# Optimization experiments

Hardware: AMD Instinct MI355X
Metric: run time of the kernel (lower is better)

Reference implementation:

```python
import jax, jax.numpy as jnp
import numpy as np


def setup_inputs() -> dict:
    key = jax.random.key(0)
    k1, k2 = jax.random.split(key)
    B, S_ENC, S_DEC, D = 8, 4096, 4096, 256
    enc_output = jax.random.normal(k1, (B, S_ENC, D), dtype=jnp.float32)
    dec_output = jax.random.normal(k2, (B, S_DEC, D), dtype=jnp.float32)
    return {"enc_output": enc_output, "dec_output": dec_output}


def reference(enc_output, dec_output):
    # a_t[b, i, j] = <enc[b, i], dec[b, j]>  -> [B, S_enc, S_dec]
    a_t = jnp.einsum('bid,bjd->bij', enc_output, dec_output)
    # softmax over encoder positions (axis=1), matching torch.softmax(a_t, dim=1)
    a_t = jax.nn.softmax(a_t, axis=1)
    # c_t[b, j, d] = sum_i a_t[b, i, j] * enc[b, i, d]  -> [B, S_dec, D]
    c_t = jnp.einsum('bij,bid->bjd', a_t, enc_output)
    return c_t
```

## Files before the change

kernel.cpp:

```cpp
#include <hip/hip_runtime.h>

typedef unsigned short u16;
typedef unsigned int u32;
typedef __attribute__((ext_vector_type(8))) _Float16 half8;
typedef __attribute__((ext_vector_type(16))) float f32x16;

#define MFMA32(A, B, C) __builtin_amdgcn_mfma_f32_32x32x16_f16(A, B, C, 0, 0, 0)

constexpr int BN = 8;
constexpr int S = 4096;
constexpr int D = 256;
constexpr int KB = 32;
constexpr int NT = S / KB;
constexpr int TILE_U16 = KB * D;

__device__ __forceinline__ u32 pk2h(float a, float b) {
  union { _Float16 h[2]; u32 u; } x;
  x.h[0] = (_Float16)a; x.h[1] = (_Float16)b;
  return x.u;
}

__device__ __forceinline__ void gload_lds16(const void* g, void* l) {
  __builtin_amdgcn_global_load_lds((__attribute__((address_space(1))) void*)(void*)g,
                                   (__attribute__((address_space(3))) void*)l, 16, 0, 0);
}

__global__ __launch_bounds__(256) void convert_enc(const float* __restrict__ enc,
                                                   u16* __restrict__ enc_ws,
                                                   u16* __restrict__ encT_ws) {
  const int blk = blockIdx.x;
  const int b = blk & 7;
  const int tp = blk >> 3;
  const int tid = threadIdx.x;

  const float* encb = enc + (size_t)b * S * D;

#pragma unroll
  for (int it = 0; it < 8; ++it) {
    int gg = it * 256 + tid;
    int t = tp * 2 + (gg >> 10);
    int g = gg & 1023;
    int i = g & 31;
    int ch = g >> 5;
    int d0 = ch * 8;
    const float* src = encb + (size_t)(t * 32 + i) * D + d0;
    float4 x = *(const float4*)src;
    float4 y = *(const float4*)(src + 4);
    uint4 o;
    o.x = pk2h(x.x, x.y); o.y = pk2h(x.z, x.w);
    o.z = pk2h(y.x, y.y); o.w = pk2h(y.z, y.w);
    *(uint4*)(enc_ws + (size_t)(b * NT + t) * TILE_U16 + g * 8) = o;
  }

  {
    int t = tp * 2 + (tid >> 7);
    int r = tid & 127;
    int o = r >> 5;
    int e = r & 31;
    int i0 = o * 8;
    int d0 = e * 8;
    float v[8][8];
#pragma unroll
    for (int rr = 0; rr < 8; ++rr) {
      const float* src = encb + (size_t)(t * 32 + i0 + rr) * D + d0;
      *(float4*)&v[rr][0] = *(const float4*)src;
      *(float4*)&v[rr][4] = *(const float4*)(src + 4);
    }
    int dsub = e >> 2;
    u16* dst = encT_ws + (size_t)(b * NT + t) * TILE_U16 + ((dsub * 4 + o) * 32 + (e & 3) * 8) * 8;
#pragma unroll
    for (int k = 0; k < 8; ++k) {
      uint4 q;
      q.x = pk2h(v[0][k], v[1][k]); q.y = pk2h(v[2][k], v[3][k]);
      q.z = pk2h(v[4][k], v[5][k]); q.w = pk2h(v[6][k], v[7][k]);
      *(uint4*)(dst + k * 8) = q;
    }
  }
}

__global__ __launch_bounds__(512, 2) void attn_kernel(const u16* __restrict__ enc_ws,
                                                      const u16* __restrict__ encT_ws,
                                                      const float* __restrict__ dec,
                                                      float* __restrict__ out) {
  __shared__ u16 lds[2][2][2 * TILE_U16];

  const int tid = threadIdx.x;
  const int w = tid >> 6;
  const int wq = w & 3;
  const int kh = w >> 2;
  const int lane = tid & 63;
  const int h = lane >> 5;
  const int l31 = lane & 31;

  const int blk = blockIdx.x;
  const int b = blk & 7;
  const int q0 = (blk >> 3) << 7;
  const int qw = q0 + wq * 32;

  const u16* encb = enc_ws + (size_t)b * NT * TILE_U16;
  const u16* encTb = encT_ws + (size_t)b * NT * TILE_U16;
  const float* decb = dec + (size_t)b * S * D;

  const float LOG2E = 1.4426950408889634f;
  half8 qf[16];
#pragma unroll
  for (int c = 0; c < 16; ++c) {
    const float* p = decb + (size_t)(qw + l31) * D + c * 16 + h * 8;
    float4 x = *(const float4*)p;
    float4 y = *(const float4*)(p + 4);
    union { u32 u[4]; half8 v; } uu;
    uu.u[0] = pk2h(x.x * LOG2E, x.y * LOG2E);
    uu.u[1] = pk2h(x.z * LOG2E, x.w * LOG2E);
    uu.u[2] = pk2h(y.x * LOG2E, y.y * LOG2E);
    uu.u[3] = pk2h(y.z * LOG2E, y.w * LOG2E);
    qf[c] = uu.v;
  }

  auto stage = [&](int buf, int t) {
    const u16* gimg = (wq < 2) ? (encb + (size_t)t * TILE_U16)
                               : (encTb + (size_t)t * TILE_U16);
    char* limg = (char*)&lds[kh][buf][(wq < 2) ? 0 : TILE_U16];
    const int half = (wq & 1) * 8192;
#pragma unroll
    for (int it = 0; it < 8; ++it) {
      int off = half + it * 1024;
      gload_lds16((const char*)gimg + off + lane * 16, limg + off);
    }
  };

  f32x16 acc[8] = {};
  float mrun = -1e30f;
  float lrun = 0.f;

  stage(0, kh);
  __syncthreads();

  for (int j = 0; j < NT / 2; ++j) {
    const int cur = j & 1;
    if (j + 1 < NT / 2) stage(cur ^ 1, 2 * (j + 1) + kh);

    f32x16 s0 = {}, s1 = {};
    const char* eb = (const char*)&lds[kh][cur][0];
#pragma unroll
    for (int c = 0; c < 16; c += 2) {
      half8 a0 = *(const half8*)(eb + ((c + 0) * 2 + h) * 512 + l31 * 16);
      half8 a1 = *(const half8*)(eb + ((c + 1) * 2 + h) * 512 + l31 * 16);
      s0 = MFMA32(a0, qf[c + 0], s0);
      s1 = MFMA32(a1, qf[c + 1], s1);
    }
    f32x16 st = s0 + s1;

    float x0 = fmaxf(st[0], st[1]), x1 = fmaxf(st[2], st[3]);
    float x2 = fmaxf(st[4], st[5]), x3 = fmaxf(st[6], st[7]);
    float x4 = fmaxf(st[8], st[9]), x5 = fmaxf(st[10], st[11]);
    float x6 = fmaxf(st[12], st[13]), x7 = fmaxf(st[14], st[15]);
    x0 = fmaxf(x0, x1); x2 = fmaxf(x2, x3); x4 = fmaxf(x4, x5); x6 = fmaxf(x6, x7);
    x0 = fmaxf(x0, x2); x4 = fmaxf(x4, x6);
    float tm = fmaxf(x0, x4);
    tm = fmaxf(tm, __shfl_xor(tm, 32));
    if (__any(tm > mrun + 11.5f)) {
      float mnew = fmaxf(mrun, tm);
      float alpha = __builtin_amdgcn_exp2f(mrun - mnew);
      mrun = mnew;
      lrun *= alpha;
#pragma unroll
      for (int ds = 0; ds < 8; ++ds)
#pragma unroll
        for (int r = 0; r < 16; ++r) acc[ds][r] *= alpha;
    }
    float p[16];
#pragma unroll
    for (int r = 0; r < 16; ++r) p[r] = __builtin_amdgcn_exp2f(st[r] - mrun);
    float y0 = (p[0] + p[1]) + (p[2] + p[3]);
    float y1 = (p[4] + p[5]) + (p[6] + p[7]);
    float y2 = (p[8] + p[9]) + (p[10] + p[11]);
    float y3 = (p[12] + p[13]) + (p[14] + p[15]);
    float rs = (y0 + y1) + (y2 + y3);
    rs += __shfl_xor(rs, 32);
    lrun += rs;

    u32 pkw[8];
#pragma unroll
    for (int rq = 0; rq < 4; ++rq) {
      pkw[rq * 2 + 0] = pk2h(p[rq * 4 + 0], p[rq * 4 + 1]);
      pkw[rq * 2 + 1] = pk2h(p[rq * 4 + 2], p[rq * 4 + 3]);
    }
    half8 bfr[2];
#pragma unroll
    for (int ic = 0; ic < 2; ++ic) {
      u32 own0 = pkw[(2 * ic + h) * 2 + 0];
      u32 own1 = pkw[(2 * ic + h) * 2 + 1];
      u32 send0 = pkw[(2 * ic + 1 - h) * 2 + 0];
      u32 send1 = pkw[(2 * ic + 1 - h) * 2 + 1];
      u32 r0 = (u32)__shfl_xor((int)send0, 32);
      u32 r1 = (u32)__shfl_xor((int)send1, 32);
      union { u32 u[4]; half8 v; } bb;
      bb.u[0] = h ? r0 : own0;
      bb.u[1] = h ? r1 : own1;
      bb.u[2] = h ? own0 : r0;
      bb.u[3] = h ? own1 : r1;
      bfr[ic] = bb.v;
    }

    const char* tb = (const char*)&lds[kh][cur][TILE_U16];
#pragma unroll
    for (int ic = 0; ic < 2; ++ic) {
#pragma unroll
      for (int ds = 0; ds < 8; ++ds) {
        half8 vf = *(const half8*)(tb + ((ds * 2 + ic) * 2 + h) * 512 + l31 * 16);
        acc[ds] = MFMA32(vf, bfr[ic], acc[ds]);
      }
    }

    __syncthreads();
  }

  float* fb = (float*)&lds[0][0][0];
  constexpr int XS = 20;
  float* mlb = fb + 30208;

  if (kh == 1) {
    if (lane < 32) {
      mlb[wq * 64 + lane] = mrun;
      mlb[wq * 64 + 32 + lane] = lrun;
    }
#pragma unroll
    for (int d4 = 0; d4 < 4; ++d4) {
      float* dst = fb + ((wq * 4 + d4) * 64 + lane) * XS;
#pragma unroll
      for (int r4 = 0; r4 < 4; ++r4) {
        float4 v;
        v.x = acc[d4][r4 * 4 + 0]; v.y = acc[d4][r4 * 4 + 1];
        v.z = acc[d4][r4 * 4 + 2]; v.w = acc[d4][r4 * 4 + 3];
        *(float4*)(dst + r4 * 4) = v;
      }
    }
  }
  __syncthreads();

  float a0 = 0.f, a1 = 0.f, inv = 0.f;
  const int q = qw + l31;
  float* orow = out + ((size_t)(b * S + q)) * D;
  if (kh == 0) {
    float m1 = mlb[wq * 64 + l31];
    float l1 = mlb[wq * 64 + 32 + l31];
    float mn = fmaxf(mrun, m1);
    a0 = __builtin_amdgcn_exp2f(mrun - mn);
    a1 = __builtin_amdgcn_exp2f(m1 - mn);
    inv = 1.0f / (a0 * lrun + a1 * l1);
#pragma unroll
    for (int d4 = 0; d4 < 4; ++d4) {
      const float* src = fb + ((wq * 4 + d4) * 64 + lane) * XS;
#pragma unroll
      for (int rq = 0; rq < 4; ++rq) {
        float4 u = *(const float4*)(src + rq * 4);
        int d = d4 * 32 + rq * 8 + h * 4;
        float4 o;
        o.x = (a0 * acc[d4][rq * 4 + 0] + a1 * u.x) * inv;
        o.y = (a0 * acc[d4][rq * 4 + 1] + a1 * u.y) * inv;
        o.z = (a0 * acc[d4][rq * 4 + 2] + a1 * u.z) * inv;
        o.w = (a0 * acc[d4][rq * 4 + 3] + a1 * u.w) * inv;
        *(float4*)(orow + d) = o;
      }
    }
  }
  __syncthreads();

  if (kh == 1) {
#pragma unroll
    for (int d4 = 0; d4 < 4; ++d4) {
      float* dst = fb + ((wq * 4 + d4) * 64 + lane) * XS;
#pragma unroll
      for (int r4 = 0; r4 < 4; ++r4) {
        float4 v;
        v.x = acc[d4 + 4][r4 * 4 + 0]; v.y = acc[d4 + 4][r4 * 4 + 1];
        v.z = acc[d4 + 4][r4 * 4 + 2]; v.w = acc[d4 + 4][r4 * 4 + 3];
        *(float4*)(dst + r4 * 4) = v;
      }
    }
  }
  __syncthreads();

  if (kh == 0) {
#pragma unroll
    for (int d4 = 0; d4 < 4; ++d4) {
      const float* src = fb + ((wq * 4 + d4) * 64 + lane) * XS;
#pragma unroll
      for (int rq = 0; rq < 4; ++rq) {
        float4 u = *(const float4*)(src + rq * 4);
        int d = (d4 + 4) * 32 + rq * 8 + h * 4;
        float4 o;
        o.x = (a0 * acc[d4 + 4][rq * 4 + 0] + a1 * u.x) * inv;
        o.y = (a0 * acc[d4 + 4][rq * 4 + 1] + a1 * u.y) * inv;
        o.z = (a0 * acc[d4 + 4][rq * 4 + 2] + a1 * u.z) * inv;
        o.w = (a0 * acc[d4 + 4][rq * 4 + 3] + a1 * u.w) * inv;
        *(float4*)(orow + d) = o;
      }
    }
  }
}

extern "C" void kernel_launch(void* const* d_in, const int* in_sizes, int n_in,
                              void* d_out, int out_size, void* d_ws, size_t ws_size,
                              hipStream_t stream) {
  const float* enc = (const float*)d_in[0];
  const float* dec = (const float*)d_in[1];
  float* out = (float*)d_out;

  u16* enc_ws = (u16*)d_ws;
  u16* encT_ws = enc_ws + (size_t)BN * NT * TILE_U16;

  convert_enc<<<BN * (S / 64), 256, 0, stream>>>(enc, enc_ws, encT_ws);
  attn_kernel<<<BN * (S / 128), 512, 0, stream>>>(enc_ws, encT_ws, dec, out);
}
```

Measured before the change: 186.9 us.

## Split key range across separate blocks with atomic-flag merge of partial softmax

```diff
diff --git a/kernel.cpp b/kernel.cpp
--- a/kernel.cpp
+++ b/kernel.cpp
@@ -13,6 +13,13 @@
 constexpr int KB = 32;
 constexpr int NT = S / KB;
 constexpr int TILE_U16 = KB * D;
+constexpr int TP_U16 = 2 * TILE_U16;
+
+constexpr size_t WS_IMG_BYTES = (size_t)BN * NT * TP_U16 * 2;
+constexpr size_t WS_ML_OFF = WS_IMG_BYTES;
+constexpr size_t WS_ML_BYTES = 256 * 128 * 8;
+constexpr size_t WS_FLAG_OFF = WS_ML_OFF + WS_ML_BYTES;
+constexpr size_t WS_NEED = WS_FLAG_OFF + 2 * 256 * 4;
 
 __device__ __forceinline__ u32 pk2h(float a, float b) {
   union { _Float16 h[2]; u32 u; } x;
@@ -26,8 +33,7 @@
 }
 
 __global__ __launch_bounds__(256) void convert_enc(const float* __restrict__ enc,
-                                                   u16* __restrict__ enc_ws,
-                                                   u16* __restrict__ encT_ws) {
+                                                   u16* __restrict__ ws) {
   const int blk = blockIdx.x;
   const int b = blk & 7;
   const int tp = blk >> 3;
@@ -49,7 +55,7 @@
     uint4 o;
     o.x = pk2h(x.x, x.y); o.y = pk2h(x.z, x.w);
     o.z = pk2h(y.x, y.y); o.w = pk2h(y.z, y.w);
-    *(uint4*)(enc_ws + (size_t)(b * NT + t) * TILE_U16 + g * 8) = o;
+    *(uint4*)(ws + (size_t)(b * NT + t) * TP_U16 + g * 8) = o;
   }
 
   {
@@ -66,8 +72,10 @@
       *(float4*)&v[rr][0] = *(const float4*)src;
       *(float4*)&v[rr][4] = *(const float4*)(src + 4);
     }
-    int dsub = e >> 2;
-    u16* dst = encT_ws + (size_t)(b * NT + t) * TILE_U16 + ((dsub * 4 + o) * 32 + (e & 3) * 8) * 8;
+    int dsub = e >> 4;
+    dsub = e >> 2;
+    u16* dst = ws + (size_t)(b * NT + t) * TP_U16 + TILE_U16 +
+               ((dsub * 4 + o) * 32 + (e & 3) * 8) * 8;
 #pragma unroll
     for (int k = 0; k < 8; ++k) {
       uint4 q;
@@ -78,27 +86,30 @@
   }
 }
 
-__global__ __launch_bounds__(512, 2) void attn_kernel(const u16* __restrict__ enc_ws,
-                                                      const u16* __restrict__ encT_ws,
-                                                      const float* __restrict__ dec,
-                                                      float* __restrict__ out) {
-  __shared__ u16 lds[2][2][2 * TILE_U16];
+__global__ __launch_bounds__(256, 2) void attn_split(const u16* __restrict__ ws_img,
+                                                     const float* __restrict__ dec,
+                                                     float* __restrict__ out,
+                                                     float2* __restrict__ mlws,
+                                                     u32* __restrict__ flag0,
+                                                     u32* __restrict__ flag1) {
+  __shared__ u16 lds2[2][TP_U16];
+  __shared__ int role_s;
 
   const int tid = threadIdx.x;
   const int w = tid >> 6;
-  const int wq = w & 3;
-  const int kh = w >> 2;
   const int lane = tid & 63;
   const int h = lane >> 5;
   const int l31 = lane & 31;
 
   const int blk = blockIdx.x;
   const int b = blk & 7;
-  const int q0 = (blk >> 3) << 7;
-  const int qw = q0 + wq * 32;
-
-  const u16* encb = enc_ws + (size_t)b * NT * TILE_U16;
-  const u16* encTb = encT_ws + (size_t)b * NT * TILE_U16;
+  const int qc = (blk >> 3) & 31;
+  const int kh = blk >> 8;
+  const int pair = blk & 255;
+  const int q0 = qc << 7;
+  const int qw = q0 + w * 32;
+
+  const char* gtile = (const char*)(ws_img + (size_t)(b * NT + kh * 64) * TP_U16);
   const float* decb = dec + (size_t)b * S * D;
 
   const float LOG2E = 1.4426950408889634f;
@@ -116,31 +127,28 @@
     qf[c] = uu.v;
   }
 
-  auto stage = [&](int buf, int t) {
-    const u16* gimg = (wq < 2) ? (encb + (size_t)t * TILE_U16)
-                               : (encTb + (size_t)t * TILE_U16);
-    char* limg = (char*)&lds[kh][buf][(wq < 2) ? 0 : TILE_U16];
-    const int half = (wq & 1) * 8192;
-#pragma unroll
-    for (int it = 0; it < 8; ++it) {
-      int off = half + it * 1024;
-      gload_lds16((const char*)gimg + off + lane * 16, limg + off);
-    }
+  auto stage = [&](int buf, size_t goff) {
+    const char* gs = gtile + goff + w * 8192 + lane * 16;
+    char* ls = (char*)&lds2[buf][0] + w * 8192;
+#pragma unroll
+    for (int it = 0; it < 8; ++it)
+      gload_lds16(gs + it * 1024, ls + it * 1024);
   };
 
   f32x16 acc[8] = {};
   float mrun = -1e30f;
   float lrun = 0.f;
 
-  stage(0, kh);
+  stage(0, 0);
   __syncthreads();
 
-  for (int j = 0; j < NT / 2; ++j) {
+  for (int j = 0; j < 64; ++j) {
     const int cur = j & 1;
-    if (j + 1 < NT / 2) stage(cur ^ 1, 2 * (j + 1) + kh);
+    if (j + 1 < 64) stage(cur ^ 1, (size_t)(j + 1) * 32768);
 
     f32x16 s0 = {}, s1 = {};
-    const char* eb = (const char*)&lds[kh][cur][0];
+    const char* eb = (const char*)&lds2[cur][0];
+    __builtin_amdgcn_s_setprio(1);
 #pragma unroll
     for (int c = 0; c < 16; c += 2) {
       half8 a0 = *(const half8*)(eb + ((c + 0) * 2 + h) * 512 + l31 * 16);
@@ -148,6 +156,7 @@
       s0 = MFMA32(a0, qf[c + 0], s0);
       s1 = MFMA32(a1, qf[c + 1], s1);
     }
+    __builtin_amdgcn_s_setprio(0);
     f32x16 st = s0 + s1;
 
     float x0 = fmaxf(st[0], st[1]), x1 = fmaxf(st[2], st[3]);
@@ -202,7 +211,197 @@
       bfr[ic] = bb.v;
     }
 
-    const char* tb = (const char*)&lds[kh][cur][TILE_U16];
+    const char* tb = (const char*)&lds2[cur][0] + TILE_U16 * 2;
+    __builtin_amdgcn_s_setprio(1);
+#pragma unroll
+    for (int ic = 0; ic < 2; ++ic) {
+#pragma unroll
+      for (int ds = 0; ds < 8; ++ds) {
+        half8 vf = *(const half8*)(tb + ((ds * 2 + ic) * 2 + h) * 512 + l31 * 16);
+        acc[ds] = MFMA32(vf, bfr[ic], acc[ds]);
+      }
+    }
+    __builtin_amdgcn_s_setprio(0);
+
+    __syncthreads();
+  }
+
+  float* orow = out + ((size_t)(b * S + qw + l31)) * D;
+
+  if (tid == 0) {
+    u32 r = __hip_atomic_fetch_add(&flag0[pair], 1u, __ATOMIC_ACQ_REL,
+                                   __HIP_MEMORY_SCOPE_AGENT);
+    role_s = (int)r;
+  }
+  __syncthreads();
+  const int role = role_s;
+
+  if (role == 0) {
+    if (lane < 32) mlws[pair * 128 + w * 32 + l31] = make_float2(mrun, lrun);
+#pragma unroll
+    for (int ds = 0; ds < 8; ++ds) {
+#pragma unroll
+      for (int rq = 0; rq < 4; ++rq) {
+        int d = ds * 32 + rq * 8 + h * 4;
+        float4 o;
+        o.x = acc[ds][rq * 4 + 0]; o.y = acc[ds][rq * 4 + 1];
+        o.z = acc[ds][rq * 4 + 2]; o.w = acc[ds][rq * 4 + 3];
+        *(float4*)(orow + d) = o;
+      }
+    }
+    __syncthreads();
+    if (tid == 0) {
+      __threadfence();
+      __hip_atomic_store(&flag1[pair], 1u, __ATOMIC_RELEASE, __HIP_MEMORY_SCOPE_AGENT);
+    }
+  } else {
+    if (tid == 0) {
+      while (__hip_atomic_load(&flag1[pair], __ATOMIC_ACQUIRE,
+                               __HIP_MEMORY_SCOPE_AGENT) == 0u)
+        __builtin_amdgcn_s_sleep(2);
+    }
+    __syncthreads();
+    float2 pml = mlws[pair * 128 + w * 32 + l31];
+    float mn = fmaxf(mrun, pml.x);
+    float a1 = __builtin_amdgcn_exp2f(mrun - mn);
+    float a0 = __builtin_amdgcn_exp2f(pml.x - mn);
+    float inv = 1.0f / (a0 * pml.y + a1 * lrun);
+#pragma unroll
+    for (int ds = 0; ds < 8; ++ds) {
+#pragma unroll
+      for (int rq = 0; rq < 4; ++rq) {
+        int d = ds * 32 + rq * 8 + h * 4;
+        float4 u = *(const float4*)(orow + d);
+        float4 o;
+        o.x = (a0 * u.x + a1 * acc[ds][rq * 4 + 0]) * inv;
+        o.y = (a0 * u.y + a1 * acc[ds][rq * 4 + 1]) * inv;
+        o.z = (a0 * u.z + a1 * acc[ds][rq * 4 + 2]) * inv;
+        o.w = (a0 * u.w + a1 * acc[ds][rq * 4 + 3]) * inv;
+        *(float4*)(orow + d) = o;
+      }
+    }
+  }
+}
+
+__global__ __launch_bounds__(512, 2) void attn_fallback(const u16* __restrict__ ws_img,
+                                                        const float* __restrict__ dec,
+                                                        float* __restrict__ out) {
+  __shared__ u16 lds[2][2][TP_U16];
+
+  const int tid = threadIdx.x;
+  const int w = tid >> 6;
+  const int wq = w & 3;
+  const int kh = w >> 2;
+  const int lane = tid & 63;
+  const int h = lane >> 5;
+  const int l31 = lane & 31;
+
+  const int blk = blockIdx.x;
+  const int b = blk & 7;
+  const int q0 = (blk >> 3) << 7;
+  const int qw = q0 + wq * 32;
+
+  const u16* packs = ws_img + (size_t)b * NT * TP_U16;
+  const float* decb = dec + (size_t)b * S * D;
+
+  const float LOG2E = 1.4426950408889634f;
+  half8 qf[16];
+#pragma unroll
+  for (int c = 0; c < 16; ++c) {
+    const float* p = decb + (size_t)(qw + l31) * D + c * 16 + h * 8;
+    float4 x = *(const float4*)p;
+    float4 y = *(const float4*)(p + 4);
+    union { u32 u[4]; half8 v; } uu;
+    uu.u[0] = pk2h(x.x * LOG2E, x.y * LOG2E);
+    uu.u[1] = pk2h(x.z * LOG2E, x.w * LOG2E);
+    uu.u[2] = pk2h(y.x * LOG2E, y.y * LOG2E);
+    uu.u[3] = pk2h(y.z * LOG2E, y.w * LOG2E);
+    qf[c] = uu.v;
+  }
+
+  auto stage = [&](int buf, int t) {
+    const char* gs = (const char*)(packs + (size_t)t * TP_U16) + wq * 8192 + lane * 16;
+    char* ls = (char*)&lds[kh][buf][0] + wq * 8192;
+#pragma unroll
+    for (int it = 0; it < 8; ++it)
+      gload_lds16(gs + it * 1024, ls + it * 1024);
+  };
+
+  f32x16 acc[8] = {};
+  float mrun = -1e30f;
+  float lrun = 0.f;
+
+  stage(0, kh);
+  __syncthreads();
+
+  for (int j = 0; j < 64; ++j) {
+    const int cur = j & 1;
+    if (j + 1 < 64) stage(cur ^ 1, 2 * (j + 1) + kh);
+
+    f32x16 s0 = {}, s1 = {};
+    const char* eb = (const char*)&lds[kh][cur][0];
+#pragma unroll
+    for (int c = 0; c < 16; c += 2) {
+      half8 a0 = *(const half8*)(eb + ((c + 0) * 2 + h) * 512 + l31 * 16);
+      half8 a1 = *(const half8*)(eb + ((c + 1) * 2 + h) * 512 + l31 * 16);
+      s0 = MFMA32(a0, qf[c + 0], s0);
+      s1 = MFMA32(a1, qf[c + 1], s1);
+    }
+    f32x16 st = s0 + s1;
+
+    float x0 = fmaxf(st[0], st[1]), x1 = fmaxf(st[2], st[3]);
+    float x2 = fmaxf(st[4], st[5]), x3 = fmaxf(st[6], st[7]);
+    float x4 = fmaxf(st[8], st[9]), x5 = fmaxf(st[10], st[11]);
+    float x6 = fmaxf(st[12], st[13]), x7 = fmaxf(st[14], st[15]);
+    x0 = fmaxf(x0, x1); x2 = fmaxf(x2, x3); x4 = fmaxf(x4, x5); x6 = fmaxf(x6, x7);
+    x0 = fmaxf(x0, x2); x4 = fmaxf(x4, x6);
+    float tm = fmaxf(x0, x4);
+    tm = fmaxf(tm, __shfl_xor(tm, 32));
+    if (__any(tm > mrun + 11.5f)) {
+      float mnew = fmaxf(mrun, tm);
+      float alpha = __builtin_amdgcn_exp2f(mrun - mnew);
+      mrun = mnew;
+      lrun *= alpha;
+#pragma unroll
+      for (int ds = 0; ds < 8; ++ds)
+#pragma unroll
+        for (int r = 0; r < 16; ++r) acc[ds][r] *= alpha;
+    }
+    float p[16];
+#pragma unroll
+    for (int r = 0; r < 16; ++r) p[r] = __builtin_amdgcn_exp2f(st[r] - mrun);
+    float y0 = (p[0] + p[1]) + (p[2] + p[3]);
+    float y1 = (p[4] + p[5]) + (p[6] + p[7]);
+    float y2 = (p[8] + p[9]) + (p[10] + p[11]);
+    float y3 = (p[12] + p[13]) + (p[14] + p[15]);
+    float rs = (y0 + y1) + (y2 + y3);
+    rs += __shfl_xor(rs, 32);
+    lrun += rs;
+
+    u32 pkw[8];
+#pragma unroll
+    for (int rq = 0; rq < 4; ++rq) {
+      pkw[rq * 2 + 0] = pk2h(p[rq * 4 + 0], p[rq * 4 + 1]);
+      pkw[rq * 2 + 1] = pk2h(p[rq * 4 + 2], p[rq * 4 + 3]);
+    }
+    half8 bfr[2];
+#pragma unroll
+    for (int ic = 0; ic < 2; ++ic) {
+      u32 own0 = pkw[(2 * ic + h) * 2 + 0];
+      u32 own1 = pkw[(2 * ic + h) * 2 + 1];
+      u32 send0 = pkw[(2 * ic + 1 - h) * 2 + 0];
+      u32 send1 = pkw[(2 * ic + 1 - h) * 2 + 1];
+      u32 r0 = (u32)__shfl_xor((int)send0, 32);
+      u32 r1 = (u32)__shfl_xor((int)send1, 32);
+      union { u32 u[4]; half8 v; } bb;
+      bb.u[0] = h ? r0 : own0;
+      bb.u[1] = h ? r1 : own1;
+      bb.u[2] = h ? own0 : r0;
+      bb.u[3] = h ? own1 : r1;
+      bfr[ic] = bb.v;
+    }
+
+    const char* tb = (const char*)&lds[kh][cur][0] + TILE_U16 * 2;
 #pragma unroll
     for (int ic = 0; ic < 2; ++ic) {
 #pragma unroll
@@ -307,9 +506,16 @@
   const float* dec = (const float*)d_in[1];
   float* out = (float*)d_out;
 
-  u16* enc_ws = (u16*)d_ws;
-  u16* encT_ws = enc_ws + (size_t)BN * NT * TILE_U16;
-
-  convert_enc<<<BN * (S / 64), 256, 0, stream>>>(enc, enc_ws, encT_ws);
-  attn_kernel<<<BN * (S / 128), 512, 0, stream>>>(enc_ws, encT_ws, dec, out);
+  u16* ws_img = (u16*)d_ws;
+
+  convert_enc<<<BN * (S / 64), 256, 0, stream>>>(enc, ws_img);
+
+  if (ws_size >= WS_NEED) {
+    float2* mlws = (float2*)((char*)d_ws + WS_ML_OFF);
+    u32* flags = (u32*)((char*)d_ws + WS_FLAG_OFF);
+    hipMemsetAsync(flags, 0, 2 * 256 * 4, stream);
+    attn_split<<<512, 256, 0, stream>>>(ws_img, dec, out, mlws, flags, flags + 256);
+  } else {
+    attn_fallback<<<BN * (S / 128), 512, 0, stream>>>(ws_img, dec, out);
+  }
 }
```

New measurement: 219.6 us. 17.5% more time.

## Ping-pong QK and softmax-PV phases between wave groups with interleaved tile layout

Applied to the files above, without the earlier changes.

```diff
diff --git a/kernel.cpp b/kernel.cpp
--- a/kernel.cpp
+++ b/kernel.cpp
@@ -3,6 +3,7 @@
 typedef unsigned short u16;
 typedef unsigned int u32;
 typedef __attribute__((ext_vector_type(8))) _Float16 half8;
+typedef __attribute__((ext_vector_type(2))) __fp16 fp16x2;
 typedef __attribute__((ext_vector_type(16))) float f32x16;
 
 #define MFMA32(A, B, C) __builtin_amdgcn_mfma_f32_32x32x16_f16(A, B, C, 0, 0, 0)
@@ -13,6 +14,7 @@
 constexpr int KB = 32;
 constexpr int NT = S / KB;
 constexpr int TILE_U16 = KB * D;
+constexpr int TP_U16 = 2 * TILE_U16;
 
 __device__ __forceinline__ u32 pk2h(float a, float b) {
   union { _Float16 h[2]; u32 u; } x;
@@ -20,14 +22,19 @@
   return x.u;
 }
 
+__device__ __forceinline__ u32 pkrtz(float a, float b) {
+  union { fp16x2 h; u32 u; } x;
+  x.h = __builtin_amdgcn_cvt_pkrtz(a, b);
+  return x.u;
+}
+
 __device__ __forceinline__ void gload_lds16(const void* g, void* l) {
   __builtin_amdgcn_global_load_lds((__attribute__((address_space(1))) void*)(void*)g,
                                    (__attribute__((address_space(3))) void*)l, 16, 0, 0);
 }
 
 __global__ __launch_bounds__(256) void convert_enc(const float* __restrict__ enc,
-                                                   u16* __restrict__ enc_ws,
-                                                   u16* __restrict__ encT_ws) {
+                                                   u16* __restrict__ ws) {
   const int blk = blockIdx.x;
   const int b = blk & 7;
   const int tp = blk >> 3;
@@ -49,7 +56,7 @@
     uint4 o;
     o.x = pk2h(x.x, x.y); o.y = pk2h(x.z, x.w);
     o.z = pk2h(y.x, y.y); o.w = pk2h(y.z, y.w);
-    *(uint4*)(enc_ws + (size_t)(b * NT + t) * TILE_U16 + g * 8) = o;
+    *(uint4*)(ws + (size_t)(b * NT + t) * TP_U16 + g * 8) = o;
   }
 
   {
@@ -67,7 +74,8 @@
       *(float4*)&v[rr][4] = *(const float4*)(src + 4);
     }
     int dsub = e >> 2;
-    u16* dst = encT_ws + (size_t)(b * NT + t) * TILE_U16 + ((dsub * 4 + o) * 32 + (e & 3) * 8) * 8;
+    u16* dst = ws + (size_t)(b * NT + t) * TP_U16 + TILE_U16 +
+               ((dsub * 4 + o) * 32 + (e & 3) * 8) * 8;
 #pragma unroll
     for (int k = 0; k < 8; ++k) {
       uint4 q;
@@ -78,11 +86,10 @@
   }
 }
 
-__global__ __launch_bounds__(512, 2) void attn_kernel(const u16* __restrict__ enc_ws,
-                                                      const u16* __restrict__ encT_ws,
+__global__ __launch_bounds__(512, 2) void attn_kernel(const u16* __restrict__ ws_img,
                                                       const float* __restrict__ dec,
                                                       float* __restrict__ out) {
-  __shared__ u16 lds[2][2][2 * TILE_U16];
+  __shared__ u16 lds[2][2][TP_U16];
 
   const int tid = threadIdx.x;
   const int w = tid >> 6;
@@ -97,8 +104,7 @@
   const int q0 = (blk >> 3) << 7;
   const int qw = q0 + wq * 32;
 
-  const u16* encb = enc_ws + (size_t)b * NT * TILE_U16;
-  const u16* encTb = encT_ws + (size_t)b * NT * TILE_U16;
+  const u16* packs = ws_img + (size_t)b * NT * TP_U16;
   const float* decb = dec + (size_t)b * S * D;
 
   const float LOG2E = 1.4426950408889634f;
@@ -116,31 +122,22 @@
     qf[c] = uu.v;
   }
 
-  auto stage = [&](int buf, int t) {
-    const u16* gimg = (wq < 2) ? (encb + (size_t)t * TILE_U16)
-                               : (encTb + (size_t)t * TILE_U16);
-    char* limg = (char*)&lds[kh][buf][(wq < 2) ? 0 : TILE_U16];
-    const int half = (wq & 1) * 8192;
-#pragma unroll
-    for (int it = 0; it < 8; ++it) {
-      int off = half + it * 1024;
-      gload_lds16((const char*)gimg + off + lane * 16, limg + off);
-    }
-  };
-
   f32x16 acc[8] = {};
   float mrun = -1e30f;
   float lrun = 0.f;
 
-  stage(0, kh);
-  __syncthreads();
-
-  for (int j = 0; j < NT / 2; ++j) {
-    const int cur = j & 1;
-    if (j + 1 < NT / 2) stage(cur ^ 1, 2 * (j + 1) + kh);
-
+  auto stagef = [&](int buf, int t) {
+    const char* gs = (const char*)(packs + (size_t)t * TP_U16) + wq * 8192 + lane * 16;
+    char* ls = (char*)&lds[kh][buf][0] + wq * 8192;
+#pragma unroll
+    for (int it = 0; it < 8; ++it)
+      gload_lds16(gs + it * 1024, ls + it * 1024);
+  };
+
+  auto qkf = [&](int buf) -> f32x16 {
     f32x16 s0 = {}, s1 = {};
-    const char* eb = (const char*)&lds[kh][cur][0];
+    const char* eb = (const char*)&lds[kh][buf][0];
+    __builtin_amdgcn_s_setprio(1);
 #pragma unroll
     for (int c = 0; c < 16; c += 2) {
       half8 a0 = *(const half8*)(eb + ((c + 0) * 2 + h) * 512 + l31 * 16);
@@ -148,15 +145,16 @@
       s0 = MFMA32(a0, qf[c + 0], s0);
       s1 = MFMA32(a1, qf[c + 1], s1);
     }
-    f32x16 st = s0 + s1;
-
-    float x0 = fmaxf(st[0], st[1]), x1 = fmaxf(st[2], st[3]);
-    float x2 = fmaxf(st[4], st[5]), x3 = fmaxf(st[6], st[7]);
-    float x4 = fmaxf(st[8], st[9]), x5 = fmaxf(st[10], st[11]);
-    float x6 = fmaxf(st[12], st[13]), x7 = fmaxf(st[14], st[15]);
-    x0 = fmaxf(x0, x1); x2 = fmaxf(x2, x3); x4 = fmaxf(x4, x5); x6 = fmaxf(x6, x7);
-    x0 = fmaxf(x0, x2); x4 = fmaxf(x4, x6);
-    float tm = fmaxf(x0, x4);
+    __builtin_amdgcn_s_setprio(0);
+    return s0 + s1;
+  };
+
+  auto smpv = [&](const f32x16& st, int buf) {
+    float x0 = fmaxf(fmaxf(st[0], st[1]), fmaxf(st[2], st[3]));
+    float x1 = fmaxf(fmaxf(st[4], st[5]), fmaxf(st[6], st[7]));
+    float x2 = fmaxf(fmaxf(st[8], st[9]), fmaxf(st[10], st[11]));
+    float x3 = fmaxf(fmaxf(st[12], st[13]), fmaxf(st[14], st[15]));
+    float tm = fmaxf(fmaxf(x0, x1), fmaxf(x2, x3));
     tm = fmaxf(tm, __shfl_xor(tm, 32));
     if (__any(tm > mrun + 11.5f)) {
       float mnew = fmaxf(mrun, tm);
@@ -182,8 +180,8 @@
     u32 pkw[8];
 #pragma unroll
     for (int rq = 0; rq < 4; ++rq) {
-      pkw[rq * 2 + 0] = pk2h(p[rq * 4 + 0], p[rq * 4 + 1]);
-      pkw[rq * 2 + 1] = pk2h(p[rq * 4 + 2], p[rq * 4 + 3]);
+      pkw[rq * 2 + 0] = pkrtz(p[rq * 4 + 0], p[rq * 4 + 1]);
+      pkw[rq * 2 + 1] = pkrtz(p[rq * 4 + 2], p[rq * 4 + 3]);
     }
     half8 bfr[2];
 #pragma unroll
@@ -202,7 +200,8 @@
       bfr[ic] = bb.v;
     }
 
-    const char* tb = (const char*)&lds[kh][cur][TILE_U16];
+    const char* tb = (const char*)&lds[kh][buf][0] + TILE_U16 * 2;
+    __builtin_amdgcn_s_setprio(1);
 #pragma unroll
     for (int ic = 0; ic < 2; ++ic) {
 #pragma unroll
@@ -211,7 +210,48 @@
         acc[ds] = MFMA32(vf, bfr[ic], acc[ds]);
       }
     }
-
+    __builtin_amdgcn_s_setprio(0);
+  };
+
+  f32x16 stp;
+
+  stagef(0, kh);
+  __syncthreads();
+
+  if (kh == 0) {
+    __syncthreads();
+    stagef(1, 2); stp = qkf(0);
+    __syncthreads();
+  } else {
+    stagef(1, 3); stp = qkf(0);
+    __syncthreads();
+    smpv(stp, 0);
+    __syncthreads();
+  }
+
+#pragma unroll 1
+  for (int j = 1; j < 64; ++j) {
+    if (kh == 0) {
+      smpv(stp, (j - 1) & 1);
+      __syncthreads();
+      if (j <= 62) stagef((j + 1) & 1, 2 * (j + 1));
+      stp = qkf(j & 1);
+      __syncthreads();
+    } else {
+      if (j <= 62) stagef((j + 1) & 1, 2 * (j + 1) + 1);
+      stp = qkf(j & 1);
+      __syncthreads();
+      smpv(stp, j & 1);
+      __syncthreads();
+    }
+  }
+
+  if (kh == 0) {
+    smpv(stp, 1);
+    __syncthreads();
+    __syncthreads();
+  } else {
+    __syncthreads();
     __syncthreads();
   }
 
@@ -307,9 +347,8 @@
   const float* dec = (const float*)d_in[1];
   float* out = (float*)d_out;
 
-  u16* enc_ws = (u16*)d_ws;
-  u16* encT_ws = enc_ws + (size_t)BN * NT * TILE_U16;
-
-  convert_enc<<<BN * (S / 64), 256, 0, stream>>>(enc, enc_ws, encT_ws);
-  attn_kernel<<<BN * (S / 128), 512, 0, stream>>>(enc_ws, encT_ws, dec, out);
-}
+  u16* ws_img = (u16*)d_ws;
+
+  convert_enc<<<BN * (S / 64), 256, 0, stream>>>(enc, ws_img);
+  attn_kernel<<<BN * (S / 128), 512, 0, stream>>>(ws_img, dec, out);
+}
```

New measurement: 215.2 us. +15.1%, slower.
